# Performance work log

Measured on AMD Instinct MI355X. Metric: run time of the kernel, lower is better.

## Reference

```python
import jax, jax.numpy as jnp
import numpy as np

B = 65536
H = W = 28
K = 3
OUT_HW = H - K + 1  # 26, valid conv
FEAT = OUT_HW * OUT_HW  # 676
HID = 200
NCLS = 10


def setup_inputs() -> dict:
    key = jax.random.key(0)
    ks = jax.random.split(key, 6)
    x = jax.random.normal(ks[0], (B, H * W), dtype=jnp.float32)
    conv_w = jnp.ones((K, K), dtype=jnp.float32)  # Parameter(ones((3,3)))
    w1 = jax.random.normal(ks[1], (FEAT, HID), dtype=jnp.float32) * (1.0 / np.sqrt(FEAT))
    b1 = jnp.zeros((HID,), dtype=jnp.float32)
    w2 = jax.random.normal(ks[2], (HID, NCLS), dtype=jnp.float32) * (1.0 / np.sqrt(HID))
    b2 = jnp.zeros((NCLS,), dtype=jnp.float32)
    return {"x": x, "conv_w": conv_w, "w1": w1, "b1": b1, "w2": w2, "b2": b2}


def _forward(x, conv_w, w1, b1, w2, b2):
    img = x.reshape(-1, H, W)  # (B,28,28)
    # valid 3x3 single-channel cross-correlation (matches input[i:i+3,j:j+3]*w)
    lhs = img[:, None, :, :]          # (B,1,28,28)
    rhs = conv_w[None, None, :, :]    # (1,1,3,3)
    conv = jax.lax.conv_general_dilated(
        lhs, rhs, window_strides=(1, 1), padding="VALID",
        dimension_numbers=("NCHW", "OIHW", "NCHW"))  # (B,1,26,26)
    feat = conv.reshape(-1, FEAT)     # (B,676)
    hidden = jax.nn.relu(feat @ w1 + b1)  # (B,200)
    return hidden @ w2 + b2               # (B,10) logits


def reference(x, conv_w, w1, b1, w2, b2):
    return _forward(x, conv_w, w1, b1, w2, b2)
```

## Files before the change

### kernel.cpp

```cpp
#include <hip/hip_runtime.h>
#include <hip/hip_bf16.h>

#define BATCH   65536
#define HW      28
#define OHW     26
#define HID     200
#define NCLS    10
#define MT2     64
#define GBLOCKS (BATCH / MT2)
#define KC32    26
#define NSTEP   13

typedef __attribute__((ext_vector_type(8))) __bf16 bf16x8;
typedef __attribute__((ext_vector_type(4))) float  f32x4;

#define KBAR() asm volatile("s_waitcnt lgkmcnt(0)\n\ts_barrier" ::: "memory")

__device__ __forceinline__ unsigned int pk2(float a, float b) {
  __hip_bfloat16 ha = __float2bfloat16(a), hb = __float2bfloat16(b);
  return (unsigned int)__builtin_bit_cast(unsigned short, ha)
       | ((unsigned int)__builtin_bit_cast(unsigned short, hb) << 16);
}

__device__ __forceinline__ uint4 pk8(float4 f0, float4 f1) {
  return make_uint4(pk2(f0.x, f0.y), pk2(f0.z, f0.w),
                    pk2(f1.x, f1.y), pk2(f1.z, f1.w));
}

__device__ __forceinline__ unsigned short* fslot(unsigned short* base, int m, int k) {
  const int kc = k >> 5;
  return base + ((kc * 64 + ((k >> 3) & 3) * 16 + (m ^ (kc & 7))) * 8) + (k & 7);
}

__global__ __launch_bounds__(256) void prep_weights(
    const float* __restrict__ w1, const float* __restrict__ cwp,
    const float* __restrict__ w2, unsigned short* __restrict__ w1e,
    unsigned short* __restrict__ w2f) {
  if (blockIdx.x < 85) {
    int c = blockIdx.x * 256 + threadIdx.x;
    if (c >= KC32 * 13 * 64) return;
    int lane = c & 63, g = c >> 6;
    int kc = g / 13, nt = g - kc * 13;
    int ln = lane & 15, qd = lane >> 4;
    int n = nt * 16 + ln;
    float cw[9];
    #pragma unroll
    for (int t = 0; t < 9; ++t) cw[t] = cwp[t];
    float v[8];
    #pragma unroll
    for (int j = 0; j < 8; ++j) {
      int k = kc * 32 + qd * 8 + j;
      float s = 0.f;
      if (k < 784 && n < HID) {
        int ri = k / 28, ci = k - ri * 28;
        #pragma unroll
        for (int di = 0; di < 3; ++di) {
          int r = ri - di;
          if (r >= 0 && r < OHW) {
            #pragma unroll
            for (int dj = 0; dj < 3; ++dj) {
              int cc = ci - dj;
              if (cc >= 0 && cc < OHW)
                s += cw[di * 3 + dj] * w1[(r * OHW + cc) * HID + n];
            }
          }
        }
      }
      v[j] = s;
    }
    *(uint4*)(w1e + (size_t)c * 8) =
        make_uint4(pk2(v[0], v[1]), pk2(v[2], v[3]),
                   pk2(v[4], v[5]), pk2(v[6], v[7]));
  } else {
    int c = (blockIdx.x - 85) * 256 + threadIdx.x;
    if (c >= 7 * 64) return;
    int lane = c & 63, kc = c >> 6;
    int col = lane & 15;
    float v[8];
    #pragma unroll
    for (int j = 0; j < 8; ++j) {
      int k = kc * 32 + (lane >> 4) * 8 + j;
      v[j] = (col < NCLS && k < HID) ? w2[k * NCLS + col] : 0.f;
    }
    *(uint4*)(w2f + (size_t)c * 8) =
        make_uint4(pk2(v[0], v[1]), pk2(v[2], v[3]),
                   pk2(v[4], v[5]), pk2(v[6], v[7]));
  }
}

template<int NT0, int NT>
__device__ __forceinline__ void gemm1_compute(
    const float* __restrict__ x, const unsigned short* __restrict__ w1e,
    unsigned short* sh, int lane, int tid, int blk64, f32x4 (&acc)[4][4]) {
  const int sc_qd = (tid >> 4) & 3;
  const float* xrow =
      x + ((size_t)blk64 + (tid >> 6) * 16 + (tid & 15)) * 784;
  const int koff = sc_qd * 8;
  const int soff = tid * 8;

  {
    float4 f0 = *(const float4*)(xrow + koff);
    float4 f1 = *(const float4*)(xrow + koff + 4);
    float4 g0 = *(const float4*)(xrow + 32 + koff);
    float4 g1 = *(const float4*)(xrow + 32 + koff + 4);
    *(uint4*)(sh + soff)        = pk8(f0, f1);
    *(uint4*)(sh + 2048 + soff) = pk8(g0, g1);
  }
  __syncthreads();

  int cur = 0;
  #pragma unroll
  for (int s = 0; s < NSTEP; ++s) {
    float4 p00, p01, p10, p11;
    const bool hav = (s + 1 < NSTEP);
    if (hav) {
      const int kb = (s + 1) * 64;
      if (s + 1 == NSTEP - 1) {
        if (sc_qd < 2) {
          p00 = *(const float4*)(xrow + 768 + koff);
          p01 = *(const float4*)(xrow + 768 + koff + 4);
        } else {
          p00 = (float4){0.f, 0.f, 0.f, 0.f};
          p01 = (float4){0.f, 0.f, 0.f, 0.f};
        }
        p10 = (float4){0.f, 0.f, 0.f, 0.f};
        p11 = (float4){0.f, 0.f, 0.f, 0.f};
      } else {
        p00 = *(const float4*)(xrow + kb + koff);
        p01 = *(const float4*)(xrow + kb + koff + 4);
        p10 = *(const float4*)(xrow + kb + 32 + koff);
        p11 = *(const float4*)(xrow + kb + 32 + koff + 4);
      }
    }

    const unsigned short* ab = sh + cur * 4096;
    #pragma unroll
    for (int h = 0; h < 2; ++h) {
      bf16x8 a[4];
      #pragma unroll
      for (int mi = 0; mi < 4; ++mi)
        a[mi] = *(const bf16x8*)(ab + h * 2048 + mi * 512 + lane * 8);
      const int kc32 = s * 2 + h;
      #pragma unroll
      for (int t = 0; t < NT; ++t) {
        bf16x8 b = *(const bf16x8*)(w1e +
                     ((size_t)(kc32 * 13 + NT0 + t) * 64 + lane) * 8);
        #pragma unroll
        for (int mi = 0; mi < 4; ++mi)
          acc[mi][t] = __builtin_amdgcn_mfma_f32_16x16x32_bf16(a[mi], b,
                                                               acc[mi][t], 0, 0, 0);
      }
    }

    if (hav) {
      unsigned short* dst = sh + (cur ^ 1) * 4096;
      *(uint4*)(dst + soff)        = pk8(p00, p01);
      *(uint4*)(dst + 2048 + soff) = pk8(p10, p11);
    }
    KBAR();
    cur ^= 1;
  }
}

template<int NT0, int NT>
__device__ __forceinline__ void gemm1_epilogue(
    const float* __restrict__ b1, unsigned short* hidA, int lane,
    f32x4 (&acc)[4][4]) {
  const int ln = lane & 15, qd = lane >> 4;
  #pragma unroll
  for (int t = 0; t < NT; ++t) {
    const int n = (NT0 + t) * 16 + ln;
    if (n < HID) {
      const float bias = b1[n];
      const int kc2 = n >> 5, qd2 = (n >> 3) & 3, j2 = n & 7, c2 = kc2 & 7;
      #pragma unroll
      for (int mi = 0; mi < 4; ++mi)
        #pragma unroll
        for (int rr = 0; rr < 4; ++rr) {
          const int m = qd * 4 + rr;
          float h = fmaxf(acc[mi][t][rr] + bias, 0.f);
          __hip_bfloat16 hb = __float2bfloat16(h);
          hidA[mi * 3584 + (kc2 * 64 + qd2 * 16 + (m ^ c2)) * 8 + j2] =
              __builtin_bit_cast(unsigned short, hb);
        }
    }
  }
}

__global__ __launch_bounds__(256, 4) void fused10(
    const float* __restrict__ x, const unsigned short* __restrict__ w1e,
    const unsigned short* __restrict__ w2f, const float* __restrict__ b1,
    const float* __restrict__ b2, float* __restrict__ out) {
  __shared__ __align__(16) unsigned short sh[4 * 3584];
  const int tid  = threadIdx.x;
  const int wave = tid >> 6;
  const int lane = tid & 63;
  const int blk64 = blockIdx.x * MT2;

  f32x4 acc[4][4];
  #pragma unroll
  for (int mi = 0; mi < 4; ++mi)
    #pragma unroll
    for (int t = 0; t < 4; ++t) acc[mi][t] = (f32x4){0.f, 0.f, 0.f, 0.f};

  switch (wave) {
    case 0:  gemm1_compute<0, 4>(x, w1e, sh, lane, tid, blk64, acc); break;
    case 1:  gemm1_compute<4, 3>(x, w1e, sh, lane, tid, blk64, acc); break;
    case 2:  gemm1_compute<7, 3>(x, w1e, sh, lane, tid, blk64, acc); break;
    default: gemm1_compute<10, 3>(x, w1e, sh, lane, tid, blk64, acc); break;
  }
  __syncthreads();

  for (int i = tid; i < 768; i += 256) {
    int mi = i / 192, r = i - mi * 192, m = r / 12, d = r - m * 12;
    *(unsigned int*)fslot(sh + mi * 3584, m, 200 + 2 * d) = 0u;
  }
  switch (wave) {
    case 0:  gemm1_epilogue<0, 4>(b1, sh, lane, acc); break;
    case 1:  gemm1_epilogue<4, 3>(b1, sh, lane, acc); break;
    case 2:  gemm1_epilogue<7, 3>(b1, sh, lane, acc); break;
    default: gemm1_epilogue<10, 3>(b1, sh, lane, acc); break;
  }
  __syncthreads();

  const int ln = lane & 15, qd = lane >> 4;
  f32x4 acc2 = (f32x4){0.f, 0.f, 0.f, 0.f};
  #pragma unroll
  for (int kc = 0; kc < 7; ++kc) {
    bf16x8 a = *(const bf16x8*)&sh[wave * 3584 + (kc * 64 + (lane ^ (kc & 7))) * 8];
    bf16x8 b = *(const bf16x8*)(w2f + ((size_t)kc * 64 + lane) * 8);
    acc2 = __builtin_amdgcn_mfma_f32_16x16x32_bf16(a, b, acc2, 0, 0, 0);
  }
  if (ln < NCLS) {
    const float bb = b2[ln];
    #pragma unroll
    for (int rr = 0; rr < 4; ++rr) {
      out[((size_t)(blockIdx.x * 4 + wave) * 16 + qd * 4 + rr) * NCLS + ln] =
          acc2[rr] + bb;
    }
  }
}

extern "C" void kernel_launch(void* const* d_in, const int* in_sizes, int n_in,
                              void* d_out, int out_size, void* d_ws, size_t ws_size,
                              hipStream_t stream) {
  const float* x  = (const float*)d_in[0];
  const float* cw = (const float*)d_in[1];
  const float* w1 = (const float*)d_in[2];
  const float* b1 = (const float*)d_in[3];
  const float* w2 = (const float*)d_in[4];
  const float* b2 = (const float*)d_in[5];
  float* out = (float*)d_out;

  unsigned short* w1e = (unsigned short*)d_ws;
  unsigned short* w2f = (unsigned short*)((char*)d_ws + 348160);

  hipLaunchKernelGGL(prep_weights, dim3(87), dim3(256), 0, stream,
                     w1, cw, w2, w1e, w2f);
  hipLaunchKernelGGL(fused10, dim3(GBLOCKS), dim3(256), 0, stream,
                     x, w1e, w2f, b1, b2, out);
}
```

Baseline: 325.6 us.

## Stage fp32 input via direct global-to-LDS loads with triple-buffered pipeline

Replaces register-staged loading of the fp32 x tile (load, convert to bf16, store to LDS) with global_load_lds DMA of raw fp32 into a 3-stage LDS ring. The bf16 conversion moves to after the LDS read. B-operand weight fragments are prefetched a step ahead in registers, and barriers use vmcnt-based partial waits. This is meant to hide global load latency and free VGPRs, at the cost of doubled LDS footprint per tile, fp32 LDS reads, and lower occupancy (launch bound 4 to 3).

```diff
diff --git a/kernel.cpp b/kernel.cpp
--- a/kernel.cpp
+++ b/kernel.cpp
@@ -14,7 +14,30 @@
 typedef __attribute__((ext_vector_type(8))) __bf16 bf16x8;
 typedef __attribute__((ext_vector_type(4))) float  f32x4;
 
-#define KBAR() asm volatile("s_waitcnt lgkmcnt(0)\n\ts_barrier" ::: "memory")
+#define STAGE16(g, l) __builtin_amdgcn_global_load_lds(                        \
+    (const __attribute__((address_space(1))) void*)(g),                        \
+    (__attribute__((address_space(3))) void*)(l), 16, 0, 0)
+
+#define FENCE() asm volatile("" ::: "memory")
+
+template<int NT> __device__ __forceinline__ void kbar_main() {
+  if constexpr (NT == 4)
+    asm volatile("s_waitcnt vmcnt(12) lgkmcnt(0)\n\ts_barrier" ::: "memory");
+  else
+    asm volatile("s_waitcnt vmcnt(10) lgkmcnt(0)\n\ts_barrier" ::: "memory");
+}
+template<int NT> __device__ __forceinline__ void kbar_tail() {
+  if constexpr (NT == 4)
+    asm volatile("s_waitcnt vmcnt(8) lgkmcnt(0)\n\ts_barrier" ::: "memory");
+  else
+    asm volatile("s_waitcnt vmcnt(6) lgkmcnt(0)\n\ts_barrier" ::: "memory");
+}
+template<int NT> __device__ __forceinline__ void kbar_pro() {
+  if constexpr (NT == 4)
+    asm volatile("s_waitcnt vmcnt(8) lgkmcnt(0)\n\ts_barrier" ::: "memory");
+  else
+    asm volatile("s_waitcnt vmcnt(7) lgkmcnt(0)\n\ts_barrier" ::: "memory");
+}
 
 __device__ __forceinline__ unsigned int pk2(float a, float b) {
   __hip_bfloat16 ha = __float2bfloat16(a), hb = __float2bfloat16(b);
@@ -91,74 +114,90 @@
 template<int NT0, int NT>
 __device__ __forceinline__ void gemm1_compute(
     const float* __restrict__ x, const unsigned short* __restrict__ w1e,
-    unsigned short* sh, int lane, int tid, int blk64, f32x4 (&acc)[4][4]) {
-  const int sc_qd = (tid >> 4) & 3;
-  const float* xrow =
-      x + ((size_t)blk64 + (tid >> 6) * 16 + (tid & 15)) * 784;
-  const int koff = sc_qd * 8;
-  const int soff = tid * 8;
-
-  {
-    float4 f0 = *(const float4*)(xrow + koff);
-    float4 f1 = *(const float4*)(xrow + koff + 4);
-    float4 g0 = *(const float4*)(xrow + 32 + koff);
-    float4 g1 = *(const float4*)(xrow + 32 + koff + 4);
-    *(uint4*)(sh + soff)        = pk8(f0, f1);
-    *(uint4*)(sh + 2048 + soff) = pk8(g0, g1);
-  }
-  __syncthreads();
-
-  int cur = 0;
+    unsigned short* sh, int lane, int wave, int blk64, f32x4 (&acc)[4][4]) {
+  const float* gsrc[4];
+  #pragma unroll
+  for (int j = 0; j < 4; ++j) {
+    const int i  = wave * 4 + j;
+    const int p  = lane & 1;
+    const int q6 = (i & 1) * 32 + (lane >> 1);
+    const int ln_ = q6 & 15, qd_ = q6 >> 4;
+    const int mi_ = (i >> 1) & 3, h_ = i >> 3;
+    gsrc[j] = x + (size_t)(blk64 + mi_ * 16 + ln_) * 784 + h_ * 32 + qd_ * 8 + p * 4;
+  }
+
+  #pragma unroll
+  for (int j = 0; j < 4; ++j) STAGE16(gsrc[j], sh + (wave * 4 + j) * 512);
+  FENCE();
+  #pragma unroll
+  for (int j = 0; j < 4; ++j) STAGE16(gsrc[j] + 64, sh + 8192 + (wave * 4 + j) * 512);
+  bf16x8 bCur[NT];
+  #pragma unroll
+  for (int t = 0; t < NT; ++t)
+    bCur[t] = *(const bf16x8*)(w1e + ((size_t)((NT0 + t) * 64 + lane)) * 8);
+  kbar_pro<NT>();
+
   #pragma unroll
   for (int s = 0; s < NSTEP; ++s) {
-    float4 p00, p01, p10, p11;
-    const bool hav = (s + 1 < NSTEP);
-    if (hav) {
-      const int kb = (s + 1) * 64;
-      if (s + 1 == NSTEP - 1) {
-        if (sc_qd < 2) {
-          p00 = *(const float4*)(xrow + 768 + koff);
-          p01 = *(const float4*)(xrow + 768 + koff + 4);
-        } else {
-          p00 = (float4){0.f, 0.f, 0.f, 0.f};
-          p01 = (float4){0.f, 0.f, 0.f, 0.f};
+    const float* af = (const float*)(const void*)sh + (s % 3) * 4096;
+
+    bf16x8 bH1[NT];
+    #pragma unroll
+    for (int t = 0; t < NT; ++t)
+      bH1[t] = *(const bf16x8*)(w1e +
+                 ((size_t)((2 * s + 1) * 13 + NT0 + t) * 64 + lane) * 8);
+    FENCE();
+    bf16x8 bNx[NT];
+    if (s + 1 < NSTEP) {
+      #pragma unroll
+      for (int t = 0; t < NT; ++t)
+        bNx[t] = *(const bf16x8*)(w1e +
+                   ((size_t)((2 * s + 2) * 13 + NT0 + t) * 64 + lane) * 8);
+    }
+    FENCE();
+    if (s + 2 < NSTEP) {
+      unsigned short* dst = sh + ((s + 2) % 3) * 8192;
+      if (s + 2 == NSTEP - 1) {
+        #pragma unroll
+        for (int j = 0; j < 4; ++j) {
+          const int off = (wave < 2 && (j & 1) == 0) ? 768 : 0;
+          STAGE16(gsrc[j] + off, dst + (wave * 4 + j) * 512);
         }
-        p10 = (float4){0.f, 0.f, 0.f, 0.f};
-        p11 = (float4){0.f, 0.f, 0.f, 0.f};
       } else {
-        p00 = *(const float4*)(xrow + kb + koff);
-        p01 = *(const float4*)(xrow + kb + koff + 4);
-        p10 = *(const float4*)(xrow + kb + 32 + koff);
-        p11 = *(const float4*)(xrow + kb + 32 + koff + 4);
+        #pragma unroll
+        for (int j = 0; j < 4; ++j)
+          STAGE16(gsrc[j] + (s + 2) * 64, dst + (wave * 4 + j) * 512);
       }
     }
-
-    const unsigned short* ab = sh + cur * 4096;
-    #pragma unroll
-    for (int h = 0; h < 2; ++h) {
-      bf16x8 a[4];
-      #pragma unroll
-      for (int mi = 0; mi < 4; ++mi)
-        a[mi] = *(const bf16x8*)(ab + h * 2048 + mi * 512 + lane * 8);
-      const int kc32 = s * 2 + h;
-      #pragma unroll
-      for (int t = 0; t < NT; ++t) {
-        bf16x8 b = *(const bf16x8*)(w1e +
-                     ((size_t)(kc32 * 13 + NT0 + t) * 64 + lane) * 8);
-        #pragma unroll
-        for (int mi = 0; mi < 4; ++mi)
-          acc[mi][t] = __builtin_amdgcn_mfma_f32_16x16x32_bf16(a[mi], b,
-                                                               acc[mi][t], 0, 0, 0);
-      }
-    }
-
-    if (hav) {
-      unsigned short* dst = sh + (cur ^ 1) * 4096;
-      *(uint4*)(dst + soff)        = pk8(p00, p01);
-      *(uint4*)(dst + 2048 + soff) = pk8(p10, p11);
-    }
-    KBAR();
-    cur ^= 1;
+    FENCE();
+
+    #pragma unroll
+    for (int mi = 0; mi < 4; ++mi) {
+      const float* ap = af + mi * 512 + lane * 8;
+      float4 v0 = *(const float4*)ap;
+      float4 v1 = *(const float4*)(ap + 4);
+      bf16x8 a = __builtin_bit_cast(bf16x8, pk8(v0, v1));
+      #pragma unroll
+      for (int t = 0; t < NT; ++t)
+        acc[mi][t] = __builtin_amdgcn_mfma_f32_16x16x32_bf16(a, bCur[t],
+                                                             acc[mi][t], 0, 0, 0);
+    }
+    #pragma unroll
+    for (int mi = 0; mi < 4; ++mi) {
+      const float* ap = af + 2048 + mi * 512 + lane * 8;
+      float4 v0 = *(const float4*)ap;
+      float4 v1 = *(const float4*)(ap + 4);
+      bf16x8 a = __builtin_bit_cast(bf16x8, pk8(v0, v1));
+      #pragma unroll
+      for (int t = 0; t < NT; ++t)
+        acc[mi][t] = __builtin_amdgcn_mfma_f32_16x16x32_bf16(a, bH1[t],
+                                                             acc[mi][t], 0, 0, 0);
+    }
+    if (s + 1 < NSTEP) {
+      #pragma unroll
+      for (int t = 0; t < NT; ++t) bCur[t] = bNx[t];
+    }
+    if (s < NSTEP - 2) kbar_main<NT>(); else kbar_tail<NT>();
   }
 }
 
@@ -187,11 +226,11 @@
   }
 }
 
-__global__ __launch_bounds__(256, 4) void fused10(
+__global__ __launch_bounds__(256, 3) void fused12(
     const float* __restrict__ x, const unsigned short* __restrict__ w1e,
     const unsigned short* __restrict__ w2f, const float* __restrict__ b1,
     const float* __restrict__ b2, float* __restrict__ out) {
-  __shared__ __align__(16) unsigned short sh[4 * 3584];
+  __shared__ __align__(16) unsigned short sh[3 * 8192];
   const int tid  = threadIdx.x;
   const int wave = tid >> 6;
   const int lane = tid & 63;
@@ -204,10 +243,10 @@
     for (int t = 0; t < 4; ++t) acc[mi][t] = (f32x4){0.f, 0.f, 0.f, 0.f};
 
   switch (wave) {
-    case 0:  gemm1_compute<0, 4>(x, w1e, sh, lane, tid, blk64, acc); break;
-    case 1:  gemm1_compute<4, 3>(x, w1e, sh, lane, tid, blk64, acc); break;
-    case 2:  gemm1_compute<7, 3>(x, w1e, sh, lane, tid, blk64, acc); break;
-    default: gemm1_compute<10, 3>(x, w1e, sh, lane, tid, blk64, acc); break;
+    case 0:  gemm1_compute<0, 4>(x, w1e, sh, lane, wave, blk64, acc); break;
+    case 1:  gemm1_compute<4, 3>(x, w1e, sh, lane, wave, blk64, acc); break;
+    case 2:  gemm1_compute<7, 3>(x, w1e, sh, lane, wave, blk64, acc); break;
+    default: gemm1_compute<10, 3>(x, w1e, sh, lane, wave, blk64, acc); break;
   }
   __syncthreads();
 
@@ -257,6 +296,6 @@
 
   hipLaunchKernelGGL(prep_weights, dim3(87), dim3(256), 0, stream,
                      w1, cw, w2, w1e, w2f);
-  hipLaunchKernelGGL(fused10, dim3(GBLOCKS), dim3(256), 0, stream,
+  hipLaunchKernelGGL(fused12, dim3(GBLOCKS), dim3(256), 0, stream,
                      x, w1e, w2f, b1, b2, out);
 }
```

Measured after the change: 318.1 us. 1.02x faster.
